# Performance work log

Measured on AMD Instinct MI355X. Metric: run time of the kernel, lower is better.

The kernel has to match this reference:

```python
import jax, jax.numpy as jnp
import numpy as np

EMB, HID, E, TOPK = 1024, 4096, 8, 2

def setup_inputs() -> dict:
    key = jax.random.key(0)
    ks = jax.random.split(key, 10)
    s = 0.02
    return {
        "x":   jax.random.normal(ks[0], (4, 2048, EMB), jnp.float32),
        # router MLP: Linear(EMB,HID) -> SiLU -> Linear(HID,E)
        "rw1": s * jax.random.normal(ks[1], (EMB, HID), jnp.float32),
        "rb1": jnp.zeros((HID,), jnp.float32),
        "rw2": s * jax.random.normal(ks[2], (HID, E), jnp.float32),
        "rb2": jnp.zeros((E,), jnp.float32),
        # stacked expert MLPs: Linear(EMB,HID) -> SiLU -> Linear(HID,EMB)
        "w1":  s * jax.random.normal(ks[3], (E, EMB, HID), jnp.float32),
        "b1":  jnp.zeros((E, HID), jnp.float32),
        "w2":  s * jax.random.normal(ks[4], (E, HID, EMB), jnp.float32),
        "b2":  jnp.zeros((E, EMB), jnp.float32),
    }

def reference(x, rw1, rb1, rw2, rb2, w1, b1, w2, b2):
    B, S, D = x.shape
    # Router: logits over experts, top-k, softmax over the k selected logits
    logits = jax.nn.silu(jnp.einsum('bsd,dh->bsh', x, rw1) + rb1)
    logits = jnp.einsum('bsh,he->bse', logits, rw2) + rb2
    k_logits, k_index = jax.lax.top_k(logits, TOPK)          # [B,S,K]
    k_prob = jax.nn.softmax(k_logits, axis=-1)               # [B,S,K]

    xf = x.reshape(B * S, D)                                 # [T,D]
    k_index_f = k_index.reshape(B * S, TOPK)
    k_prob_f = k_prob.reshape(B * S, TOPK)

    out = jnp.zeros_like(xf)
    for e in range(E):  # small fixed expert count
        # per-token combine weight for expert e (0 if not routed)
        we = jnp.sum(jnp.where(k_index_f == e, k_prob_f, 0.0), axis=-1)  # [T]
        h = jax.nn.silu(xf @ w1[e] + b1[e]) @ w2[e] + b2[e]              # [T,D]
        out = out + we[:, None] * h
    return out.reshape(B, S, D)
```

## Files before the change

### kernel.cpp

```cpp
#include <hip/hip_runtime.h>
#include <stdint.h>

#define TOK 8192
#define EMBD 1024
#define HIDD 4096
#define NEXP 8

typedef _Float16 f16;
typedef _Float16 f16x8 __attribute__((ext_vector_type(8)));
typedef _Float16 f16x4 __attribute__((ext_vector_type(4)));
typedef float f32x4 __attribute__((ext_vector_type(4)));
typedef unsigned short u16;
typedef unsigned short u16x4 __attribute__((ext_vector_type(4)));

constexpr size_t OFF_X16   = 0;
constexpr size_t OFF_RW1T  = OFF_X16  + (size_t)TOK*EMBD*2;
constexpr size_t OFF_W1T   = OFF_RW1T + (size_t)HIDD*EMBD*2;
constexpr size_t OFF_W2T   = OFF_W1T  + (size_t)NEXP*HIDD*EMBD*2;
constexpr size_t OFF_HR    = OFF_W2T  + (size_t)NEXP*EMBD*HIDD*2;
constexpr size_t OFF_HG    = OFF_HR   + (size_t)TOK*HIDD*2;
constexpr size_t OFF_YG    = OFF_HG   + (size_t)(2*TOK+256)*HIDD*2;
constexpr size_t OFF_XF    = OFF_YG   + (size_t)(2*TOK+256)*EMBD*2;
constexpr size_t OFF_HF    = OFF_XF   + 512UL*EMBD*4;
constexpr size_t OFF_KIDX  = OFF_HF   + 512UL*HIDD*4;
constexpr size_t OFF_KW    = OFF_KIDX + 2UL*TOK*4;
constexpr size_t OFF_RMAP  = OFF_KW   + 2UL*TOK*4;
constexpr size_t OFF_TMAP  = OFF_RMAP + 2UL*TOK*4;
constexpr size_t OFF_FLAG  = OFF_TMAP + 2UL*TOK*4;
constexpr size_t OFF_MISC  = OFF_FLAG + 512UL*4;
constexpr size_t WS_TOTAL  = OFF_MISC + 1024;

__device__ __align__(1024) unsigned char g_ws[WS_TOTAL];

__device__ __forceinline__ u16 f2h(float f) {
  f16 h = (f16)f;
  return __builtin_bit_cast(u16, h);
}

__device__ __forceinline__ void async_cp16(const void* g, void* l) {
  __builtin_amdgcn_global_load_lds((const __attribute__((address_space(1))) void*)g,
                                   (__attribute__((address_space(3))) void*)l, 16, 0, 0);
}

__global__ void k_init() {
  int* misc = (int*)(g_ws + OFF_MISC);
  if (threadIdx.x < 32) misc[threadIdx.x] = 0;
}

__global__ void k_cvt_x(const float* __restrict__ x) {
  u16* X16 = (u16*)(g_ws + OFF_X16);
  int i = (blockIdx.x * 256 + threadIdx.x) * 4;
  float4 v = *(const float4*)(x + i);
  u16x4 o;
  o[0] = f2h(v.x); o[1] = f2h(v.y); o[2] = f2h(v.z); o[3] = f2h(v.w);
  *(u16x4*)(X16 + i) = o;
}

__global__ void k_transpose(const float* __restrict__ in, size_t offOut, int R, int C) {
  u16* out = (u16*)(g_ws + offOut);
  __shared__ u16 t[64][68];
  int r0 = blockIdx.y * 64, c0 = blockIdx.x * 64;
  size_t mb = (size_t)blockIdx.z * R * C;
  in += mb; out += mb;
  int tid = threadIdx.x;
#pragma unroll
  for (int i = 0; i < 4; ++i) {
    int r = i * 16 + (tid >> 4);
    int c4 = (tid & 15) * 4;
    float4 v = *(const float4*)&in[(size_t)(r0 + r) * C + c0 + c4];
    u16x4 p;
    p[0] = f2h(v.x); p[1] = f2h(v.y); p[2] = f2h(v.z); p[3] = f2h(v.w);
    *(u16x4*)&t[r][c4] = p;
  }
  __syncthreads();
#pragma unroll
  for (int i = 0; i < 4; ++i) {
    int lin = i * 256 + tid;
    int cc = lin >> 4;
    int rr0 = (lin & 15) * 4;
    u16x4 o;
    o[0] = t[rr0 + 0][cc];
    o[1] = t[rr0 + 1][cc];
    o[2] = t[rr0 + 2][cc];
    o[3] = t[rr0 + 3][cc];
    *(u16x4*)&out[(size_t)(c0 + cc) * R + r0 + rr0] = o;
  }
}

template <bool SILU, bool GROUPED, bool INDIRECT, int GN>
__global__ __launch_bounds__(512, 2) void gemm256(size_t offA, size_t offB,
                                                  const float* __restrict__ bias,
                                                  size_t offC, int Mfix, int N, int K) {
  const u16* A  = (const u16*)(g_ws + offA);
  const u16* BT = (const u16*)(g_ws + offB);
  u16* C = (u16*)(g_ws + offC);
  const int* offs = (const int*)(g_ws + OFF_MISC) + 8;
  const int* tokmap = (const int*)(g_ws + OFF_TMAP);

  int nx = gridDim.x, ny = gridDim.y;
  int nwg = nx * ny * gridDim.z;
  int flat = (blockIdx.z * ny + blockIdx.y) * nx + blockIdx.x;
  int cpx = nwg >> 3;
  int u = (flat & 7) * cpx + (flat >> 3);
  int bxin = u % GN;
  int t1 = u / GN;
  int by = t1 % ny;
  int t2 = t1 / ny;
  int nxg = nx / GN;
  int g = t2 % nxg;
  int bz = t2 / nxg;
  int bx = g * GN + bxin;

  int e = GROUPED ? bz : 0;
  int rbase = GROUPED ? offs[e] : 0;
  int Me = GROUPED ? (offs[e + 1] - rbase) : Mfix;
  int m0 = by * 256;
  if (m0 >= Me) return;
  int n0 = bx * 256;
  const u16* Be = BT + (size_t)e * N * K;
  const float* be = bias + (size_t)e * N;

  __shared__ __align__(128) u16 SM[65536];

  int tid = threadIdx.x;
  int lane = tid & 63, wid = tid >> 6;
  int wm = wid >> 2, wn = wid & 3;
  int rsel = lane & 15;
  int rg = lane >> 4;
  int sp0 = (rg ^ (rsel & 7)) * 8;

  int srow = tid >> 3;
  int cnom = tid & 7;
  int csrc = (cnom ^ (srow & 7)) * 8;

  const u16* aP[4];
  const u16* bP[4];
#pragma unroll
  for (int i = 0; i < 4; ++i) {
    int r = m0 + i * 64 + srow;
    if (GROUPED) r = (r < Me) ? r : (Me - 1);
    if (INDIRECT) aP[i] = A + (size_t)tokmap[rbase + r] * K + csrc;
    else          aP[i] = A + (size_t)(rbase + r) * K + csrc;
    bP[i] = Be + (size_t)(n0 + i * 64 + srow) * K + csrc;
  }

#define STAGE(b, k0)                                                        \
  do {                                                                      \
    _Pragma("unroll") for (int i = 0; i < 4; ++i)                           \
      async_cp16(aP[i] + (k0), &SM[(b)*16384 + (i * 512 + tid) * 8]);       \
    _Pragma("unroll") for (int i = 0; i < 4; ++i)                           \
      async_cp16(bP[i] + (k0), &SM[32768 + (b)*16384 + (i * 512 + tid) * 8]); \
  } while (0)

#define COMPUTE(bb)                                                             \
  {                                                                             \
    const u16* Ab = &SM[(bb)*16384];                                            \
    const u16* Bb = &SM[32768 + (bb)*16384];                                    \
    _Pragma("unroll") for (int ks = 0; ks < 2; ++ks) {                          \
      int spo = sp0 ^ (ks << 5);                                                \
      f16x8 af[8], bf[4];                                                       \
      _Pragma("unroll") for (int i = 0; i < 8; ++i)                             \
        af[i] = *(const f16x8*)&Ab[wm * 8192 + i * 1024 + rsel * 64 + spo];     \
      _Pragma("unroll") for (int j = 0; j < 4; ++j)                             \
        bf[j] = *(const f16x8*)&Bb[wn * 4096 + j * 1024 + rsel * 64 + spo];     \
      _Pragma("unroll") for (int i = 0; i < 8; ++i)                             \
        _Pragma("unroll") for (int j = 0; j < 4; ++j)                           \
          acc[i][j] = __builtin_amdgcn_mfma_f32_16x16x32_f16(af[i], bf[j],      \
                                                             acc[i][j], 0, 0, 0); \
    }                                                                           \
  }

  f32x4 acc[8][4] = {};
  int nt = K >> 6;

  STAGE(0, 0);
  asm volatile("s_waitcnt vmcnt(0)" ::: "memory");
  __builtin_amdgcn_s_barrier();

  int buf = 0;
  for (int t = 0; t < nt; ++t) {
    if (t + 1 < nt) STAGE(buf ^ 1, (t + 1) << 6);
    COMPUTE(buf);
    asm volatile("s_waitcnt vmcnt(0)" ::: "memory");
    __builtin_amdgcn_s_barrier();
    buf ^= 1;
  }
#undef COMPUTE
#undef STAGE

  u16* Cs = SM;
#pragma unroll
  for (int j = 0; j < 4; ++j) {
    int colL = wn * 64 + j * 16 + rsel;
    float bn = be[n0 + colL];
#pragma unroll
    for (int i = 0; i < 8; ++i) {
#pragma unroll
      for (int r = 0; r < 4; ++r) {
        int ml = wm * 128 + i * 16 + rg * 4 + r;
        float v = acc[i][j][r] + bn;
        if (SILU) v = v / (1.0f + __expf(-v));
        Cs[ml * 256 + colL] = f2h(v);
      }
    }
  }
  __syncthreads();
#pragma unroll
  for (int i = 0; i < 16; ++i) {
    int lin = i * 512 + tid;
    int row = lin >> 5, sl = lin & 31;
    if (!GROUPED || (m0 + row < Me))
      *(uint4*)(C + (size_t)(rbase + m0 + row) * N + n0 + sl * 8) =
          *(const uint4*)&Cs[row * 256 + sl * 8];
  }
}

__global__ void k_router(const float* __restrict__ rw2, const float* __restrict__ rb2,
                         const float* __restrict__ x) {
  const u16* HR = (const u16*)(g_ws + OFF_HR);
  int* kidx = (int*)(g_ws + OFF_KIDX);
  float* kw = (float*)(g_ws + OFF_KW);
  int* flag = (int*)(g_ws + OFF_FLAG);
  float* XF = (float*)(g_ws + OFF_XF);
  int* misc = (int*)(g_ws + OFF_MISC);

  int t = blockIdx.x, tid = threadIdx.x;
  int lane = tid & 63, w = tid >> 6;
  float acc[8] = {};
  const u16* hrow = HR + (size_t)t * HIDD;
#pragma unroll
  for (int i = 0; i < 2; ++i) {
    int base = i * 2048 + tid * 8;
    f16x8 v = *(const f16x8*)&hrow[base];
#pragma unroll
    for (int jj = 0; jj < 8; ++jj) {
      float hv = (float)v[jj];
      const float* r2 = rw2 + (size_t)(base + jj) * 8;
#pragma unroll
      for (int e2 = 0; e2 < 8; ++e2) acc[e2] += hv * r2[e2];
    }
  }
#pragma unroll
  for (int m = 1; m < 64; m <<= 1)
#pragma unroll
    for (int e2 = 0; e2 < 8; ++e2) acc[e2] += __shfl_xor(acc[e2], m);

  __shared__ float red[4][8];
  __shared__ int s_fi;
  if (lane == 0)
    for (int e2 = 0; e2 < 8; ++e2) red[w][e2] = acc[e2];
  if (tid == 0) s_fi = -1;
  __syncthreads();
  if (tid == 0) {
    float lg[8];
    for (int e2 = 0; e2 < 8; ++e2)
      lg[e2] = red[0][e2] + red[1][e2] + red[2][e2] + red[3][e2] + rb2[e2];
    int i1 = 0; float l1 = lg[0];
    for (int e2 = 1; e2 < 8; ++e2) if (lg[e2] > l1) { l1 = lg[e2]; i1 = e2; }
    int i2 = -1; float l2 = -3.4e38f;
    for (int e2 = 0; e2 < 8; ++e2) if (e2 != i1 && lg[e2] > l2) { l2 = lg[e2]; i2 = e2; }
    float l3 = -3.4e38f;
    for (int e2 = 0; e2 < 8; ++e2) if (e2 != i1 && e2 != i2 && lg[e2] > l3) l3 = lg[e2];
    float ex = __expf(l2 - l1);
    float inv = 1.0f / (1.0f + ex);
    kidx[2 * t] = i1; kidx[2 * t + 1] = i2;
    kw[2 * t] = inv;  kw[2 * t + 1] = ex * inv;
    if (l2 - l3 < 4e-3f) {
      int fi = atomicAdd(misc + 30, 1);
      if (fi < 512) { flag[fi] = t; s_fi = fi; }
    }
  }
  __syncthreads();
  int fi = s_fi;
  if (fi >= 0) {
    const float* xs = x + (size_t)t * EMBD;
    float* xd = XF + (size_t)fi * EMBD;
    int d = tid * 4;
    *(float4*)(xd + d) = *(const float4*)(xs + d);
  }
}

__global__ __launch_bounds__(256) void k_flag_gemm(const float* __restrict__ rw1,
                                                   const float* __restrict__ rb1) {
  int* misc = (int*)(g_ws + OFF_MISC);
  int F = misc[30]; if (F > 512) F = 512;
  int m0 = blockIdx.y * 64;
  if (m0 >= F) return;
  int n0 = blockIdx.x * 64;
  const float* XF = (const float*)(g_ws + OFF_XF);
  float* HF = (float*)(g_ws + OFF_HF);
  __shared__ float As[64][17];
  __shared__ float Bs[16][65];
  int tid = threadIdx.x;
  float acc[4][4] = {};
  for (int k0 = 0; k0 < EMBD; k0 += 16) {
#pragma unroll
    for (int i = 0; i < 4; ++i) {
      int lin = i * 256 + tid;
      As[lin >> 4][lin & 15] = XF[(size_t)(m0 + (lin >> 4)) * EMBD + k0 + (lin & 15)];
      Bs[lin >> 6][lin & 63] = rw1[(size_t)(k0 + (lin >> 6)) * HIDD + n0 + (lin & 63)];
    }
    __syncthreads();
    int ty = tid >> 4, tx = tid & 15;
#pragma unroll
    for (int kk = 0; kk < 16; ++kk) {
      float a4[4], b4[4];
#pragma unroll
      for (int a = 0; a < 4; ++a) a4[a] = As[ty * 4 + a][kk];
#pragma unroll
      for (int b = 0; b < 4; ++b) b4[b] = Bs[kk][tx * 4 + b];
#pragma unroll
      for (int a = 0; a < 4; ++a)
#pragma unroll
        for (int b = 0; b < 4; ++b) acc[a][b] += a4[a] * b4[b];
    }
    __syncthreads();
  }
  int ty = tid >> 4, tx = tid & 15;
  for (int a = 0; a < 4; ++a)
    for (int b = 0; b < 4; ++b) {
      int n = n0 + tx * 4 + b;
      float v = acc[a][b] + rb1[n];
      v = v / (1.0f + __expf(-v));
      HF[(size_t)(m0 + ty * 4 + a) * HIDD + n] = v;
    }
}

__global__ void k_flag_fix(const float* __restrict__ rw2, const float* __restrict__ rb2) {
  int* misc = (int*)(g_ws + OFF_MISC);
  int F = misc[30]; if (F > 512) F = 512;
  int fi = blockIdx.x; if (fi >= F) return;
  const int* flag = (const int*)(g_ws + OFF_FLAG);
  const float* HF = (const float*)(g_ws + OFF_HF);
  int* kidx = (int*)(g_ws + OFF_KIDX);
  float* kw = (float*)(g_ws + OFF_KW);
  int t = flag[fi];
  int tid = threadIdx.x, lane = tid & 63, w = tid >> 6;
  const float* h = HF + (size_t)fi * HIDD;
  float acc[8] = {};
  for (int i = 0; i < 16; ++i) {
    int hh = i * 256 + tid;
    float hv = h[hh];
    const float* r2 = rw2 + (size_t)hh * 8;
#pragma unroll
    for (int e2 = 0; e2 < 8; ++e2) acc[e2] += hv * r2[e2];
  }
#pragma unroll
  for (int m = 1; m < 64; m <<= 1)
#pragma unroll
    for (int e2 = 0; e2 < 8; ++e2) acc[e2] += __shfl_xor(acc[e2], m);
  __shared__ float red[4][8];
  if (lane == 0)
    for (int e2 = 0; e2 < 8; ++e2) red[w][e2] = acc[e2];
  __syncthreads();
  if (tid == 0) {
    float lg[8];
    for (int e2 = 0; e2 < 8; ++e2)
      lg[e2] = red[0][e2] + red[1][e2] + red[2][e2] + red[3][e2] + rb2[e2];
    int i1 = 0; float l1 = lg[0];
    for (int e2 = 1; e2 < 8; ++e2) if (lg[e2] > l1) { l1 = lg[e2]; i1 = e2; }
    int i2 = -1; float l2 = -3.4e38f;
    for (int e2 = 0; e2 < 8; ++e2) if (e2 != i1 && lg[e2] > l2) { l2 = lg[e2]; i2 = e2; }
    float ex = __expf(l2 - l1);
    float inv = 1.0f / (1.0f + ex);
    kidx[2 * t] = i1; kidx[2 * t + 1] = i2;
    kw[2 * t] = inv;  kw[2 * t + 1] = ex * inv;
  }
}

__global__ void k_count() {
  int idx = blockIdx.x * 256 + threadIdx.x;
  if (idx < 2 * TOK) {
    int* misc = (int*)(g_ws + OFF_MISC);
    const int* kidx = (const int*)(g_ws + OFF_KIDX);
    atomicAdd(&misc[kidx[idx]], 1);
  }
}

__global__ void k_scan() {
  if (threadIdx.x == 0) {
    int* misc = (int*)(g_ws + OFF_MISC);
    int* counts = misc; int* offs = misc + 8; int* cur = misc + 20;
    offs[0] = 0;
    for (int e = 0; e < 8; ++e) { offs[e + 1] = offs[e] + counts[e]; cur[e] = offs[e]; }
  }
}

__global__ void k_build() {
  int s = blockIdx.x * 256 + threadIdx.x;
  if (s < 2 * TOK) {
    const int* kidx = (const int*)(g_ws + OFF_KIDX);
    int* rowmap = (int*)(g_ws + OFF_RMAP);
    int* tokmap = (int*)(g_ws + OFF_TMAP);
    int* misc = (int*)(g_ws + OFF_MISC);
    int e = kidx[s];
    int r = atomicAdd(&misc[20 + e], 1);
    rowmap[s] = r;
    tokmap[r] = s >> 1;
  }
}

__global__ void k_combine(float* __restrict__ out) {
  int t = blockIdx.x, tid = threadIdx.x;
  const int* rowmap = (const int*)(g_ws + OFF_RMAP);
  const float* kw = (const float*)(g_ws + OFF_KW);
  const u16* YG = (const u16*)(g_ws + OFF_YG);
  int r0 = rowmap[2 * t], r1 = rowmap[2 * t + 1];
  float w0 = kw[2 * t], w1 = kw[2 * t + 1];
  int d = tid * 4;
  f16x4 a = *(const f16x4*)(YG + (size_t)r0 * EMBD + d);
  f16x4 b = *(const f16x4*)(YG + (size_t)r1 * EMBD + d);
  float4 o;
  o.x = w0 * (float)a[0] + w1 * (float)b[0];
  o.y = w0 * (float)a[1] + w1 * (float)b[1];
  o.z = w0 * (float)a[2] + w1 * (float)b[2];
  o.w = w0 * (float)a[3] + w1 * (float)b[3];
  *(float4*)(out + (size_t)t * EMBD + d) = o;
}

extern "C" void kernel_launch(void* const* d_in, const int* in_sizes, int n_in,
                              void* d_out, int out_size, void* d_ws, size_t ws_size,
                              hipStream_t stream) {
  const float* x   = (const float*)d_in[0];
  const float* rw1 = (const float*)d_in[1];
  const float* rb1 = (const float*)d_in[2];
  const float* rw2 = (const float*)d_in[3];
  const float* rb2 = (const float*)d_in[4];
  const float* w1  = (const float*)d_in[5];
  const float* b1  = (const float*)d_in[6];
  const float* w2  = (const float*)d_in[7];
  const float* b2  = (const float*)d_in[8];
  float* out = (float*)d_out;

  k_init<<<dim3(1), dim3(32), 0, stream>>>();
  k_cvt_x<<<dim3(TOK * EMBD / 1024), dim3(256), 0, stream>>>(x);
  k_transpose<<<dim3(HIDD / 64, EMBD / 64, 1), dim3(256), 0, stream>>>(rw1, OFF_RW1T, EMBD, HIDD);
  k_transpose<<<dim3(HIDD / 64, EMBD / 64, 8), dim3(256), 0, stream>>>(w1, OFF_W1T, EMBD, HIDD);
  k_transpose<<<dim3(EMBD / 64, HIDD / 64, 8), dim3(256), 0, stream>>>(w2, OFF_W2T, HIDD, EMBD);
  gemm256<true, false, false, 4><<<dim3(HIDD / 256, TOK / 256, 1), dim3(512), 0, stream>>>(
      OFF_X16, OFF_RW1T, rb1, OFF_HR, TOK, HIDD, EMBD);
  k_router<<<dim3(TOK), dim3(256), 0, stream>>>(rw2, rb2, x);
  k_flag_gemm<<<dim3(HIDD / 64, 8), dim3(256), 0, stream>>>(rw1, rb1);
  k_flag_fix<<<dim3(512), dim3(256), 0, stream>>>(rw2, rb2);
  k_count<<<dim3(2 * TOK / 256), dim3(256), 0, stream>>>();
  k_scan<<<dim3(1), dim3(1), 0, stream>>>();
  k_build<<<dim3(2 * TOK / 256), dim3(256), 0, stream>>>();
  gemm256<true, true, true, 4><<<dim3(HIDD / 256, 2 * TOK / 256, 8), dim3(512), 0, stream>>>(
      OFF_X16, OFF_W1T, b1, OFF_HG, 0, HIDD, EMBD);
  gemm256<false, true, false, 1><<<dim3(EMBD / 256, 2 * TOK / 256, 8), dim3(512), 0, stream>>>(
      OFF_HG, OFF_W2T, b2, OFF_YG, 0, EMBD, HIDD);
  k_combine<<<dim3(TOK), dim3(256), 0, stream>>>(out);
}
```

Baseline: 983.2 us.

## Interleave async prefetch with MFMA in four sub-phases using ping-pong barriers

Splits each K-tile's compute into four sub-phases. Each sub-phase loads a slice of A fragments from LDS, issues part of the next tile's global-to-LDS copies, and runs its MFMAs under raised wave priority, with scheduling barriers and block barriers between phases. The aim is to spread global loads and LDS reads across the MFMA stream so the matrix units are not stalled behind one bulk stage per iteration. The cost is eight extra block barriers per K tile, plus a register-pressure risk from holding all B fragments for both k-steps at once.

```diff
diff --git a/kernel.cpp b/kernel.cpp
--- a/kernel.cpp
+++ b/kernel.cpp
@@ -152,24 +152,6 @@
       async_cp16(bP[i] + (k0), &SM[32768 + (b)*16384 + (i * 512 + tid) * 8]); \
   } while (0)
 
-#define COMPUTE(bb)                                                             \
-  {                                                                             \
-    const u16* Ab = &SM[(bb)*16384];                                            \
-    const u16* Bb = &SM[32768 + (bb)*16384];                                    \
-    _Pragma("unroll") for (int ks = 0; ks < 2; ++ks) {                          \
-      int spo = sp0 ^ (ks << 5);                                                \
-      f16x8 af[8], bf[4];                                                       \
-      _Pragma("unroll") for (int i = 0; i < 8; ++i)                             \
-        af[i] = *(const f16x8*)&Ab[wm * 8192 + i * 1024 + rsel * 64 + spo];     \
-      _Pragma("unroll") for (int j = 0; j < 4; ++j)                             \
-        bf[j] = *(const f16x8*)&Bb[wn * 4096 + j * 1024 + rsel * 64 + spo];     \
-      _Pragma("unroll") for (int i = 0; i < 8; ++i)                             \
-        _Pragma("unroll") for (int j = 0; j < 4; ++j)                           \
-          acc[i][j] = __builtin_amdgcn_mfma_f32_16x16x32_f16(af[i], bf[j],      \
-                                                             acc[i][j], 0, 0, 0); \
-    }                                                                           \
-  }
-
   f32x4 acc[8][4] = {};
   int nt = K >> 6;
 
@@ -177,17 +159,58 @@
   asm volatile("s_waitcnt vmcnt(0)" ::: "memory");
   __builtin_amdgcn_s_barrier();
 
-  int buf = 0;
   for (int t = 0; t < nt; ++t) {
-    if (t + 1 < nt) STAGE(buf ^ 1, (t + 1) << 6);
-    COMPUTE(buf);
-    asm volatile("s_waitcnt vmcnt(0)" ::: "memory");
-    __builtin_amdgcn_s_barrier();
-    buf ^= 1;
-  }
-#undef COMPUTE
+    int b = t & 1;
+    const u16* Ab = &SM[b * 16384];
+    const u16* Bb = &SM[32768 + b * 16384];
+    bool pf = (t + 1 < nt);
+    int k1 = (t + 1) << 6;
+    f16x8 bf[4][2];
+
+#pragma unroll
+    for (int q = 0; q < 4; ++q) {
+      f16x8 af[2][2];
+#pragma unroll
+      for (int dm = 0; dm < 2; ++dm)
+#pragma unroll
+        for (int ks = 0; ks < 2; ++ks)
+          af[dm][ks] = *(const f16x8*)&Ab[wm * 8192 + (q * 2 + dm) * 1024 +
+                                          rsel * 64 + (sp0 ^ (ks << 5))];
+      if (q == 0) {
+#pragma unroll
+        for (int j = 0; j < 4; ++j)
+#pragma unroll
+          for (int ks = 0; ks < 2; ++ks)
+            bf[j][ks] = *(const f16x8*)&Bb[wn * 4096 + j * 1024 +
+                                           rsel * 64 + (sp0 ^ (ks << 5))];
+      }
+      if (pf) {
+        async_cp16(aP[q] + k1, &SM[(b ^ 1) * 16384 + (q * 512 + tid) * 8]);
+        async_cp16(bP[q] + k1, &SM[32768 + (b ^ 1) * 16384 + (q * 512 + tid) * 8]);
+      }
+      __builtin_amdgcn_s_barrier();
+      asm volatile("s_waitcnt lgkmcnt(0)" ::: "memory");
+      __builtin_amdgcn_sched_barrier(0);
+      __builtin_amdgcn_s_setprio(1);
+#pragma unroll
+      for (int dm = 0; dm < 2; ++dm)
+#pragma unroll
+        for (int j = 0; j < 4; ++j)
+#pragma unroll
+          for (int ks = 0; ks < 2; ++ks)
+            acc[q * 2 + dm][j] = __builtin_amdgcn_mfma_f32_16x16x32_f16(
+                af[dm][ks], bf[j][ks], acc[q * 2 + dm][j], 0, 0, 0);
+      __builtin_amdgcn_s_setprio(0);
+      __builtin_amdgcn_sched_barrier(0);
+      if (q == 3) {
+        asm volatile("s_waitcnt vmcnt(0)" ::: "memory");
+      }
+      __builtin_amdgcn_s_barrier();
+    }
+  }
 #undef STAGE
 
+  __syncthreads();
   u16* Cs = SM;
 #pragma unroll
   for (int j = 0; j < 4; ++j) {
```

Result: slower. 1.069 ms (+8.8%).
